# Optimization experiments

Hardware: AMD Instinct MI355X
Metric: run time of the kernel (lower is better)

## Reference

```python
import jax, jax.numpy as jnp
import numpy as np

HEAD_SIZE = 64
N_EMBED = 768
B, T = 16, 2048


def setup_inputs() -> dict:
    key = jax.random.key(0)
    ks = jax.random.split(key, 7)
    return {
        "x": jax.random.normal(ks[0], (B, T, N_EMBED), dtype=jnp.float32),
        "v1": jax.random.normal(ks[1], (B, T, HEAD_SIZE), dtype=jnp.float32),
        "Wk": jax.random.normal(ks[2], (N_EMBED, HEAD_SIZE), dtype=jnp.float32) * 0.02,
        "Wq": jax.random.normal(ks[3], (N_EMBED, HEAD_SIZE), dtype=jnp.float32) * 0.02,
        "Wv": jax.random.normal(ks[4], (N_EMBED, HEAD_SIZE), dtype=jnp.float32) * 0.02,
        "Wproj": jax.random.normal(ks[5], (HEAD_SIZE, HEAD_SIZE), dtype=jnp.float32) * 0.02,
        "bproj": jnp.zeros((HEAD_SIZE,), dtype=jnp.float32),
        "lamb": jnp.float32(0.5),
    }


def reference(x, v1, Wk, Wq, Wv, Wproj, bproj, lamb):
    # x: [B, T, C]; single-head causal attention with value-residual mixing.
    k = x @ Wk  # [B, T, H]
    q = x @ Wq
    v = x @ Wv
    v = (1.0 - lamb) * v + lamb * v1  # value-residual mix
    scale = jnp.float32(1.0 / np.sqrt(HEAD_SIZE))
    w = jnp.einsum("bth,bsh->bts", q, k) * scale  # [B, T, T]
    t = x.shape[1]
    causal = jnp.tril(jnp.ones((t, t), dtype=bool))  # [T, T]
    w = jnp.where(causal, w, jnp.float32(-jnp.inf))
    w = jax.nn.softmax(w, axis=-1)
    # dropout is identity in eval mode
    out = jnp.einsum("bts,bsh->bth", w, v)  # [B, T, H]
    return out @ Wproj + bproj, v1
```

## Files before the change

kernel.cpp:

```cpp
#include <hip/hip_runtime.h>
#include <hip/hip_bf16.h>


constexpr int BATCH = 16;
constexpr int TSEQ  = 2048;
constexpr int CEMB  = 768;
constexpr int HS    = 64;
constexpr size_t NTOK    = (size_t)BATCH * TSEQ;
constexpr size_t OUTHALF = NTOK * HS;

typedef __bf16 bf16x4 __attribute__((ext_vector_type(4)));
typedef __bf16 bf16x8 __attribute__((ext_vector_type(8)));
typedef float  f32x4  __attribute__((ext_vector_type(4)));
typedef float  f32x16 __attribute__((ext_vector_type(16)));
typedef int    i32x4  __attribute__((ext_vector_type(4)));

__global__ __launch_bounds__(256) void prep_kernel(
    const float* __restrict__ wk, const float* __restrict__ wq,
    const float* __restrict__ wv, const float* __restrict__ wproj,
    __bf16* __restrict__ wt, __bf16* __restrict__ wpt)
{
    __shared__ __bf16 t[64][66];
    const int bid = blockIdx.x;
    if (bid < 36) {
        const int m = bid / 12, c0 = (bid % 12) * 64;
        const float* src = (m == 0) ? wk : (m == 1) ? wq : wv;
        for (int i = threadIdx.x; i < 4096; i += 256) {
            const int c = i >> 6, h = i & 63;
            t[c][h] = (__bf16)src[(size_t)(c0 + c) * HS + h];
        }
        __syncthreads();
        for (int i = threadIdx.x; i < 4096; i += 256) {
            const int h = i >> 6, c = i & 63;
            wt[(size_t)m * HS * CEMB + (size_t)h * CEMB + c0 + c] = t[c][h];
        }
    } else {
        for (int i = threadIdx.x; i < 4096; i += 256) {
            const int h = i >> 6, hp = i & 63;
            t[h][hp] = (__bf16)wproj[i];
        }
        __syncthreads();
        for (int i = threadIdx.x; i < 4096; i += 256) {
            const int hp = i >> 6, h = i & 63;
            wpt[i] = t[h][hp];
        }
    }
}

__global__ __launch_bounds__(256, 2) void qkv_kernel(
    const float* __restrict__ x,
    const float* __restrict__ v1,
    const __bf16* __restrict__ wt,
    const float* __restrict__ lamb_p,
    __bf16* __restrict__ kk,
    __bf16* __restrict__ qq,
    __bf16* __restrict__ vt,
    float* __restrict__ v1out)
{
    __shared__ __bf16 xl[2][64][88];

    const int wave = threadIdx.x >> 6;
    const int lane = threadIdx.x & 63;
    const int l16  = lane & 15;
    const int quad = lane >> 4;
    const size_t row0 = (size_t)blockIdx.x * 64;

    const int tok_s = threadIdx.x >> 2;
    const int cq    = threadIdx.x & 3;
    const float* xsrc = x + (row0 + tok_s) * CEMB + cq * 16;

    const __bf16* wbase[3];
    #pragma unroll
    for (int m = 0; m < 3; ++m)
        wbase[m] = wt + ((size_t)m * HS + wave * 16 + l16) * CEMB + quad * 8;

    f32x4 acc[3][4];
    #pragma unroll
    for (int m = 0; m < 3; ++m)
        #pragma unroll
        for (int rt = 0; rt < 4; ++rt)
            acc[m][rt] = (f32x4){0.f, 0.f, 0.f, 0.f};

    auto issueX = [&](int chunk, f32x4& a0, f32x4& a1, f32x4& a2, f32x4& a3) {
        const float* xs = xsrc + chunk * 64;
        a0 = *(const f32x4*)(xs);
        a1 = *(const f32x4*)(xs + 4);
        a2 = *(const f32x4*)(xs + 8);
        a3 = *(const f32x4*)(xs + 12);
    };
    auto writeX = [&](int buf, const f32x4& a0, const f32x4& a1,
                      const f32x4& a2, const f32x4& a3) {
        bf16x8 lo, hi;
        #pragma unroll
        for (int i = 0; i < 4; ++i) {
            lo[i] = (__bf16)a0[i]; lo[i + 4] = (__bf16)a1[i];
            hi[i] = (__bf16)a2[i]; hi[i + 4] = (__bf16)a3[i];
        }
        *(bf16x8*)&xl[buf][tok_s][cq * 16]     = lo;
        *(bf16x8*)&xl[buf][tok_s][cq * 16 + 8] = hi;
    };
    auto loadW = [&](int chunk, bf16x8 (&w)[3][2]) {
        #pragma unroll
        for (int m = 0; m < 3; ++m)
            #pragma unroll
            for (int ks = 0; ks < 2; ++ks)
                w[m][ks] = *(const bf16x8*)(wbase[m] + chunk * 64 + ks * 32);
    };
    auto compute = [&](int buf, const bf16x8 (&w)[3][2]) {
        #pragma unroll
        for (int ks = 0; ks < 2; ++ks) {
            bf16x8 a[4];
            #pragma unroll
            for (int rt = 0; rt < 4; ++rt)
                a[rt] = *(const bf16x8*)&xl[buf][rt * 16 + l16][ks * 32 + quad * 8];
            #pragma unroll
            for (int m = 0; m < 3; ++m)
                #pragma unroll
                for (int rt = 0; rt < 4; ++rt)
                    acc[m][rt] = __builtin_amdgcn_mfma_f32_16x16x32_bf16(
                        a[rt], w[m][ks], acc[m][rt], 0, 0, 0);
        }
    };

    f32x4 xa0, xa1, xa2, xa3, xb0, xb1, xb2, xb3;
    {
        f32x4 t0, t1, t2, t3;
        issueX(0, t0, t1, t2, t3);
        writeX(0, t0, t1, t2, t3);
    }
    issueX(1, xa0, xa1, xa2, xa3);
    issueX(2, xb0, xb1, xb2, xb3);
    bf16x8 wcur[3][2], wnxt[3][2];
    loadW(0, wcur);
    __syncthreads();

    constexpr int NCH = CEMB / 64;
    #pragma unroll
    for (int ci = 0; ci < NCH; ci += 2) {
        loadW(ci + 1, wnxt);
        compute(0, wcur);
        writeX(1, xa0, xa1, xa2, xa3);
        if (ci + 3 < NCH) issueX(ci + 3, xa0, xa1, xa2, xa3);
        __syncthreads();

        if (ci + 2 < NCH) loadW(ci + 2, wcur);
        compute(1, wnxt);
        if (ci + 2 < NCH) {
            writeX(0, xb0, xb1, xb2, xb3);
            if (ci + 4 < NCH) issueX(ci + 4, xb0, xb1, xb2, xb3);
            __syncthreads();
        }
    }

    const float lam = lamb_p[0];
    const int col = wave * 16 + l16;
    const int b  = (int)(row0 >> 11);
    __bf16* vtb = vt + (size_t)b * HS * TSEQ + (size_t)col * TSEQ;
    #pragma unroll
    for (int rt = 0; rt < 4; ++rt) {
        const size_t tok0 = row0 + rt * 16 + quad * 4;
        bf16x4 pk;
        #pragma unroll
        for (int r = 0; r < 4; ++r) {
            const size_t idx = (tok0 + r) * HS + col;
            const float v1v = v1[idx];
            kk[idx] = (__bf16)acc[0][rt][r];
            qq[idx] = (__bf16)acc[1][rt][r];
            pk[r] = (__bf16)((1.0f - lam) * acc[2][rt][r] + lam * v1v);
            if (v1out) v1out[idx] = v1v;
        }
        *(bf16x4*)(vtb + (tok0 & 2047)) = pk;
    }
}

__device__ __forceinline__ int pk2(float lo, float hi) {
    unsigned short a = __builtin_bit_cast(unsigned short, (__bf16)lo);
    unsigned short b = __builtin_bit_cast(unsigned short, (__bf16)hi);
    return (int)((((unsigned)b) << 16) | (unsigned)a);
}
__device__ __forceinline__ bf16x8 make_bfrag(const float* p, int hi) {
    const int a0 = pk2(p[0], p[1]), a1 = pk2(p[2], p[3]);
    const int b0 = pk2(p[4], p[5]), b1 = pk2(p[6], p[7]);
    const int pa0 = __shfl_xor(a0, 32), pa1 = __shfl_xor(a1, 32);
    const int pb0 = __shfl_xor(b0, 32), pb1 = __shfl_xor(b1, 32);
    i32x4 w;
    w[0] = hi ? pb0 : a0;
    w[1] = hi ? pb1 : a1;
    w[2] = hi ? b0  : pa0;
    w[3] = hi ? b1  : pa1;
    return __builtin_bit_cast(bf16x8, w);
}

__global__ __launch_bounds__(256, 2) void attn_kernel(
    const __bf16* __restrict__ q,
    const __bf16* __restrict__ k,
    const __bf16* __restrict__ vt,
    const __bf16* __restrict__ wpt,
    const float* __restrict__ bproj,
    float* __restrict__ y)
{
    __shared__ float olds[4][64][32];
    __shared__ float mred[4][32];
    __shared__ float lred[4][32];

    const int b    = blockIdx.x >> 5;
    const int jp   = blockIdx.x & 31;
    const int wave = threadIdx.x >> 6;
    const int lane = threadIdx.x & 63;
    const int l31  = lane & 31;
    const int hi   = lane >> 5;
    const int hi8  = hi * 8;

    const __bf16* kb = k  + (size_t)b * TSEQ * HS;
    const __bf16* vb = vt + (size_t)b * HS * TSEQ;
    const float sc2 = 0.125f * 1.44269504f;

    bf16x8 wf[4];
    if (wave < 2) {
        const __bf16* wp = wpt + (size_t)(wave * 32 + l31) * HS + hi8;
        #pragma unroll
        for (int c = 0; c < 4; ++c) wf[c] = *(const bf16x8*)(wp + c * 16);
    }

    for (int pass = 0; pass < 2; ++pass) {
        const int j = pass ? (63 - jp) : jp;
        const size_t tok0 = (size_t)b * TSEQ + (size_t)j * 32;

        const __bf16* qp = q + (tok0 + l31) * HS + hi8;
        bf16x8 qf[4];
        #pragma unroll
        for (int c = 0; c < 4; ++c) qf[c] = *(const bf16x8*)(qp + c * 16);

        f32x16 o0, o1;
        #pragma unroll
        for (int r = 0; r < 16; ++r) { o0[r] = 0.f; o1[r] = 0.f; }
        float m_i = -1e30f, l_i = 0.f;

        bf16x8 kf[4], kn[4];
        if (wave <= j) {
            const __bf16* kp = kb + (size_t)(wave * 32 + l31) * HS + hi8;
            #pragma unroll
            for (int c = 0; c < 4; ++c) kf[c] = *(const bf16x8*)(kp + c * 16);
        }

        for (int t = wave; t <= j; t += 4) {
            const int s0 = t * 32;
            bf16x8 vf[4];
            #pragma unroll
            for (int ht = 0; ht < 2; ++ht)
                #pragma unroll
                for (int c2 = 0; c2 < 2; ++c2)
                    vf[ht * 2 + c2] = *(const bf16x8*)(vb
                        + (size_t)(ht * 32 + l31) * TSEQ + s0 + c2 * 16 + hi8);
            if (t + 4 <= j) {
                const __bf16* kp = kb + (size_t)((t + 4) * 32 + l31) * HS + hi8;
                #pragma unroll
                for (int c = 0; c < 4; ++c) kn[c] = *(const bf16x8*)(kp + c * 16);
            }

            f32x16 s;
            #pragma unroll
            for (int r = 0; r < 16; ++r) s[r] = 0.f;
            #pragma unroll
            for (int c = 0; c < 4; ++c)
                s = __builtin_amdgcn_mfma_f32_32x32x16_bf16(kf[c], qf[c], s, 0, 0, 0);

            float p[16];
            if (t == j) {
                #pragma unroll
                for (int r = 0; r < 16; ++r) {
                    const int krow = (r & 3) + 8 * (r >> 2) + 4 * hi;
                    p[r] = (krow <= l31) ? s[r] * sc2 : -1e30f;
                }
            } else {
                #pragma unroll
                for (int r = 0; r < 16; ++r) p[r] = s[r] * sc2;
            }

            float x0 = fmaxf(p[0], p[1]),   x1 = fmaxf(p[2], p[3]);
            float x2 = fmaxf(p[4], p[5]),   x3 = fmaxf(p[6], p[7]);
            float x4 = fmaxf(p[8], p[9]),   x5 = fmaxf(p[10], p[11]);
            float x6 = fmaxf(p[12], p[13]), x7 = fmaxf(p[14], p[15]);
            float mx = fmaxf(fmaxf(fmaxf(x0, x1), fmaxf(x2, x3)),
                             fmaxf(fmaxf(x4, x5), fmaxf(x6, x7)));
            mx = fmaxf(mx, __shfl_xor(mx, 32));

            if (!__all(mx <= m_i + 8.f)) {
                const float mn = fmaxf(m_i, mx);
                const float alpha = exp2f(m_i - mn);
                m_i = mn;
                l_i *= alpha;
                #pragma unroll
                for (int r = 0; r < 16; ++r) { o0[r] *= alpha; o1[r] *= alpha; }
            }

            #pragma unroll
            for (int r = 0; r < 16; ++r) p[r] = exp2f(p[r] - m_i);

            float r0 = (p[0] + p[1]) + (p[2] + p[3]);
            float r1 = (p[4] + p[5]) + (p[6] + p[7]);
            float r2 = (p[8] + p[9]) + (p[10] + p[11]);
            float r3 = (p[12] + p[13]) + (p[14] + p[15]);
            float rs = (r0 + r1) + (r2 + r3);
            rs += __shfl_xor(rs, 32);
            l_i += rs;

            const bf16x8 fb0 = make_bfrag(&p[0], hi);
            const bf16x8 fb1 = make_bfrag(&p[8], hi);

            o0 = __builtin_amdgcn_mfma_f32_32x32x16_bf16(vf[0], fb0, o0, 0, 0, 0);
            o0 = __builtin_amdgcn_mfma_f32_32x32x16_bf16(vf[1], fb1, o0, 0, 0, 0);
            o1 = __builtin_amdgcn_mfma_f32_32x32x16_bf16(vf[2], fb0, o1, 0, 0, 0);
            o1 = __builtin_amdgcn_mfma_f32_32x32x16_bf16(vf[3], fb1, o1, 0, 0, 0);

            if (t + 4 <= j) {
                #pragma unroll
                for (int c = 0; c < 4; ++c) kf[c] = kn[c];
            }
        }

        #pragma unroll
        for (int r = 0; r < 16; ++r) {
            const int row = (r & 3) + 8 * (r >> 2) + 4 * hi;
            olds[wave][row][l31]      = o0[r];
            olds[wave][row + 32][l31] = o1[r];
        }
        if (lane < 32) { mred[wave][lane] = m_i; lred[wave][lane] = l_i; }
        __syncthreads();

        if (wave < 2) {
            float mw[4], lw[4];
            #pragma unroll
            for (int w = 0; w < 4; ++w) { mw[w] = mred[w][l31]; lw[w] = lred[w][l31]; }
            const float mg = fmaxf(fmaxf(mw[0], mw[1]), fmaxf(mw[2], mw[3]));
            float g[4], lg = 0.f;
            #pragma unroll
            for (int w = 0; w < 4; ++w) { g[w] = exp2f(mw[w] - mg); lg += g[w] * lw[w]; }
            const float inv = 1.0f / lg;

            float on[32];
            #pragma unroll
            for (int r = 0; r < 16; ++r) {
                const int row = (r & 3) + 8 * (r >> 2) + 4 * hi;
                float a0 = 0.f, a1 = 0.f;
                #pragma unroll
                for (int w = 0; w < 4; ++w) {
                    a0 += g[w] * olds[w][row][l31];
                    a1 += g[w] * olds[w][row + 32][l31];
                }
                on[r]      = a0 * inv;
                on[r + 16] = a1 * inv;
            }

            f32x16 res;
            #pragma unroll
            for (int r = 0; r < 16; ++r) res[r] = 0.f;
            #pragma unroll
            for (int c = 0; c < 4; ++c) {
                const bf16x8 ob = make_bfrag(&on[c * 8], hi);
                res = __builtin_amdgcn_mfma_f32_32x32x16_bf16(wf[c], ob, res, 0, 0, 0);
            }

            float* yp = y + (tok0 + l31) * HS + wave * 32;
            #pragma unroll
            for (int grp = 0; grp < 4; ++grp) {
                const f32x4 bb = *(const f32x4*)(bproj + wave * 32 + grp * 8 + 4 * hi);
                f32x4 o4;
                #pragma unroll
                for (int rr = 0; rr < 4; ++rr) o4[rr] = res[grp * 4 + rr] + bb[rr];
                *(f32x4*)(yp + grp * 8 + 4 * hi) = o4;
            }
        }
        __syncthreads();
    }
}

__global__ __launch_bounds__(256) void copy_kernel(
    const float* __restrict__ src, float* __restrict__ dst)
{
    const size_t i = ((size_t)blockIdx.x * 256 + threadIdx.x) * 4;
    *(f32x4*)(dst + i) = *(const f32x4*)(src + i);
}

extern "C" void kernel_launch(void* const* d_in, const int* in_sizes, int n_in,
                              void* d_out, int out_size, void* d_ws, size_t ws_size,
                              hipStream_t stream) {
    const float* x     = (const float*)d_in[0];
    const float* v1    = (const float*)d_in[1];
    const float* wk    = (const float*)d_in[2];
    const float* wq    = (const float*)d_in[3];
    const float* wv    = (const float*)d_in[4];
    const float* wproj = (const float*)d_in[5];
    const float* bproj = (const float*)d_in[6];
    const float* lamb  = (const float*)d_in[7];

    float* out = (float*)d_out;

    __bf16* qp  = (__bf16*)d_ws;
    __bf16* wt  = qp + OUTHALF;
    __bf16* wpt = wt + (size_t)3 * HS * CEMB;
    const size_t base_elems = OUTHALF + (size_t)3 * HS * CEMB + (size_t)HS * HS;
    const size_t need_bytes = (base_elems + 2 * OUTHALF) * sizeof(__bf16);

    __bf16* kp;
    __bf16* vtp;
    float*  v1out;
    const bool fused_v1 = (ws_size >= need_bytes);
    if (fused_v1) {
        kp    = wpt + (size_t)HS * HS;
        vtp   = kp + OUTHALF;
        v1out = out + OUTHALF;
    } else {
        kp    = (__bf16*)(out + OUTHALF);
        vtp   = kp + OUTHALF;
        v1out = nullptr;
    }

    prep_kernel<<<dim3(37), dim3(256), 0, stream>>>(wk, wq, wv, wproj, wt, wpt);

    qkv_kernel<<<dim3((int)(NTOK / 64)), dim3(256), 0, stream>>>(
        x, v1, wt, lamb, kp, qp, vtp, v1out);

    attn_kernel<<<dim3(BATCH * 32), dim3(256), 0, stream>>>(
        qp, kp, vtp, wpt, bproj, out);

    if (!fused_v1) {
        copy_kernel<<<dim3((int)(OUTHALF / (256 * 4))), dim3(256), 0, stream>>>(
            v1, out + OUTHALF);
    }
}
```

Before: 229.4 us.

## Split QKV projection across grid.y so each block computes one matrix

The QKV projection kernel launches three blocks per 64-token tile, one each for K, Q and V, instead of one block computing all three. This cuts accumulator and weight registers so the launch bound can allow four blocks per CU, and the x pipeline becomes a simpler single-stage double buffer. In exchange, the fp32 x activations are read and converted three times instead of once, which raises global memory traffic unless the cache absorbs the repeats.

Result: slower. 250.0 us (+9.0%).

```diff
diff --git a/kernel.cpp b/kernel.cpp
--- a/kernel.cpp
+++ b/kernel.cpp
@@ -47,7 +47,7 @@
     }
 }
 
-__global__ __launch_bounds__(256, 2) void qkv_kernel(
+__global__ __launch_bounds__(256, 4) void qkv_kernel(
     const float* __restrict__ x,
     const float* __restrict__ v1,
     const __bf16* __restrict__ wt,
@@ -59,6 +59,7 @@
 {
     __shared__ __bf16 xl[2][64][88];
 
+    const int mm   = blockIdx.y;
     const int wave = threadIdx.x >> 6;
     const int lane = threadIdx.x & 63;
     const int l16  = lane & 15;
@@ -69,17 +70,11 @@
     const int cq    = threadIdx.x & 3;
     const float* xsrc = x + (row0 + tok_s) * CEMB + cq * 16;
 
-    const __bf16* wbase[3];
+    const __bf16* wb = wt + ((size_t)mm * HS + wave * 16 + l16) * CEMB + quad * 8;
+
+    f32x4 acc[4];
     #pragma unroll
-    for (int m = 0; m < 3; ++m)
-        wbase[m] = wt + ((size_t)m * HS + wave * 16 + l16) * CEMB + quad * 8;
-
-    f32x4 acc[3][4];
-    #pragma unroll
-    for (int m = 0; m < 3; ++m)
-        #pragma unroll
-        for (int rt = 0; rt < 4; ++rt)
-            acc[m][rt] = (f32x4){0.f, 0.f, 0.f, 0.f};
+    for (int rt = 0; rt < 4; ++rt) acc[rt] = (f32x4){0.f, 0.f, 0.f, 0.f};
 
     auto issueX = [&](int chunk, f32x4& a0, f32x4& a1, f32x4& a2, f32x4& a3) {
         const float* xs = xsrc + chunk * 64;
@@ -99,77 +94,84 @@
         *(bf16x8*)&xl[buf][tok_s][cq * 16]     = lo;
         *(bf16x8*)&xl[buf][tok_s][cq * 16 + 8] = hi;
     };
-    auto loadW = [&](int chunk, bf16x8 (&w)[3][2]) {
-        #pragma unroll
-        for (int m = 0; m < 3; ++m)
-            #pragma unroll
-            for (int ks = 0; ks < 2; ++ks)
-                w[m][ks] = *(const bf16x8*)(wbase[m] + chunk * 64 + ks * 32);
-    };
-    auto compute = [&](int buf, const bf16x8 (&w)[3][2]) {
-        #pragma unroll
-        for (int ks = 0; ks < 2; ++ks) {
-            bf16x8 a[4];
-            #pragma unroll
-            for (int rt = 0; rt < 4; ++rt)
-                a[rt] = *(const bf16x8*)&xl[buf][rt * 16 + l16][ks * 32 + quad * 8];
-            #pragma unroll
-            for (int m = 0; m < 3; ++m)
-                #pragma unroll
-                for (int rt = 0; rt < 4; ++rt)
-                    acc[m][rt] = __builtin_amdgcn_mfma_f32_16x16x32_bf16(
-                        a[rt], w[m][ks], acc[m][rt], 0, 0, 0);
-        }
-    };
-
-    f32x4 xa0, xa1, xa2, xa3, xb0, xb1, xb2, xb3;
+
     {
         f32x4 t0, t1, t2, t3;
         issueX(0, t0, t1, t2, t3);
         writeX(0, t0, t1, t2, t3);
     }
+    f32x4 xa0, xa1, xa2, xa3;
     issueX(1, xa0, xa1, xa2, xa3);
-    issueX(2, xb0, xb1, xb2, xb3);
-    bf16x8 wcur[3][2], wnxt[3][2];
-    loadW(0, wcur);
+    bf16x8 wc0 = *(const bf16x8*)(wb);
+    bf16x8 wc1 = *(const bf16x8*)(wb + 32);
     __syncthreads();
 
     constexpr int NCH = CEMB / 64;
     #pragma unroll
-    for (int ci = 0; ci < NCH; ci += 2) {
-        loadW(ci + 1, wnxt);
-        compute(0, wcur);
-        writeX(1, xa0, xa1, xa2, xa3);
-        if (ci + 3 < NCH) issueX(ci + 3, xa0, xa1, xa2, xa3);
-        __syncthreads();
-
-        if (ci + 2 < NCH) loadW(ci + 2, wcur);
-        compute(1, wnxt);
-        if (ci + 2 < NCH) {
-            writeX(0, xb0, xb1, xb2, xb3);
-            if (ci + 4 < NCH) issueX(ci + 4, xb0, xb1, xb2, xb3);
+    for (int ci = 0; ci < NCH; ++ci) {
+        const int buf = ci & 1;
+        const bool notlast = (ci + 1 < NCH);
+
+        bf16x8 wn0, wn1;
+        if (notlast) {
+            wn0 = *(const bf16x8*)(wb + (ci + 1) * 64);
+            wn1 = *(const bf16x8*)(wb + (ci + 1) * 64 + 32);
+        }
+
+        #pragma unroll
+        for (int ks = 0; ks < 2; ++ks) {
+            const bf16x8 w = ks ? wc1 : wc0;
+            #pragma unroll
+            for (int rt = 0; rt < 4; ++rt) {
+                const bf16x8 a = *(const bf16x8*)
+                    &xl[buf][rt * 16 + l16][ks * 32 + quad * 8];
+                acc[rt] = __builtin_amdgcn_mfma_f32_16x16x32_bf16(
+                    a, w, acc[rt], 0, 0, 0);
+            }
+        }
+
+        if (notlast) {
+            writeX(buf ^ 1, xa0, xa1, xa2, xa3);
+            if (ci + 2 < NCH) issueX(ci + 2, xa0, xa1, xa2, xa3);
+            wc0 = wn0; wc1 = wn1;
             __syncthreads();
         }
     }
 
-    const float lam = lamb_p[0];
     const int col = wave * 16 + l16;
-    const int b  = (int)(row0 >> 11);
-    __bf16* vtb = vt + (size_t)b * HS * TSEQ + (size_t)col * TSEQ;
-    #pragma unroll
-    for (int rt = 0; rt < 4; ++rt) {
-        const size_t tok0 = row0 + rt * 16 + quad * 4;
-        bf16x4 pk;
-        #pragma unroll
-        for (int r = 0; r < 4; ++r) {
-            const size_t idx = (tok0 + r) * HS + col;
-            const float v1v = v1[idx];
-            kk[idx] = (__bf16)acc[0][rt][r];
-            qq[idx] = (__bf16)acc[1][rt][r];
-            pk[r] = (__bf16)((1.0f - lam) * acc[2][rt][r] + lam * v1v);
-            if (v1out) v1out[idx] = v1v;
-        }
-        *(bf16x4*)(vtb + (tok0 & 2047)) = pk;
+    if (mm == 0) {
+        #pragma unroll
+        for (int rt = 0; rt < 4; ++rt) {
+            const size_t tok0 = row0 + rt * 16 + quad * 4;
+            #pragma unroll
+            for (int r = 0; r < 4; ++r)
+                kk[(tok0 + r) * HS + col] = (__bf16)acc[rt][r];
+        }
+    } else if (mm == 1) {
+        #pragma unroll
+        for (int rt = 0; rt < 4; ++rt) {
+            const size_t tok0 = row0 + rt * 16 + quad * 4;
+            #pragma unroll
+            for (int r = 0; r < 4; ++r)
+                qq[(tok0 + r) * HS + col] = (__bf16)acc[rt][r];
+        }
+    } else {
+        const float lam = lamb_p[0];
+        const int b = (int)(row0 >> 11);
+        __bf16* vtb = vt + (size_t)b * HS * TSEQ + (size_t)col * TSEQ;
+        #pragma unroll
+        for (int rt = 0; rt < 4; ++rt) {
+            const size_t tok0 = row0 + rt * 16 + quad * 4;
+            bf16x4 pk;
+            #pragma unroll
+            for (int r = 0; r < 4; ++r) {
+                const size_t idx = (tok0 + r) * HS + col;
+                const float v1v = v1[idx];
+                pk[r] = (__bf16)((1.0f - lam) * acc[rt][r] + lam * v1v);
+                if (v1out) v1out[idx] = v1v;
+            }
+            *(bf16x4*)(vtb + (tok0 & 2047)) = pk;
+        }
     }
 }
 
@@ -418,7 +420,7 @@
 
     prep_kernel<<<dim3(37), dim3(256), 0, stream>>>(wk, wq, wv, wproj, wt, wpt);
 
-    qkv_kernel<<<dim3((int)(NTOK / 64)), dim3(256), 0, stream>>>(
+    qkv_kernel<<<dim3((int)(NTOK / 64), 3), dim3(256), 0, stream>>>(
         x, v1, wt, lamb, kp, qp, vtp, v1out);
 
     attn_kernel<<<dim3(BATCH * 32), dim3(256), 0, stream>>>(
```

## Stage x tiles into LDS with direct global_load_lds in the QKV projection

Applied to the files above, without the earlier changes.

The QKV projection kernel now copies fp32 x chunks straight from global memory into shared memory using global_load_lds, rather than loading into registers, converting to bf16 and storing to LDS. The bf16 conversion moves to the point where MFMA operands are read from LDS. The pipeline becomes a double buffer with one chunk per iteration and a single sync, which frees registers and removes the register round trip. In exchange the LDS footprint doubles because fp32 is stored, LDS read traffic doubles, and conversion work is repeated on every operand read.

Result: no change. 228.0 us (-0.6%).

```diff
diff --git a/kernel.cpp b/kernel.cpp
--- a/kernel.cpp
+++ b/kernel.cpp
@@ -57,7 +57,7 @@
     __bf16* __restrict__ vt,
     float* __restrict__ v1out)
 {
-    __shared__ __bf16 xl[2][64][88];
+    __shared__ float xf[2][64][68];
 
     const int wave = threadIdx.x >> 6;
     const int lane = threadIdx.x & 63;
@@ -65,10 +65,6 @@
     const int quad = lane >> 4;
     const size_t row0 = (size_t)blockIdx.x * 64;
 
-    const int tok_s = threadIdx.x >> 2;
-    const int cq    = threadIdx.x & 3;
-    const float* xsrc = x + (row0 + tok_s) * CEMB + cq * 16;
-
     const __bf16* wbase[3];
     #pragma unroll
     for (int m = 0; m < 3; ++m)
@@ -81,23 +77,16 @@
         for (int rt = 0; rt < 4; ++rt)
             acc[m][rt] = (f32x4){0.f, 0.f, 0.f, 0.f};
 
-    auto issueX = [&](int chunk, f32x4& a0, f32x4& a1, f32x4& a2, f32x4& a3) {
-        const float* xs = xsrc + chunk * 64;
-        a0 = *(const f32x4*)(xs);
-        a1 = *(const f32x4*)(xs + 4);
-        a2 = *(const f32x4*)(xs + 8);
-        a3 = *(const f32x4*)(xs + 12);
-    };
-    auto writeX = [&](int buf, const f32x4& a0, const f32x4& a1,
-                      const f32x4& a2, const f32x4& a3) {
-        bf16x8 lo, hi;
-        #pragma unroll
-        for (int i = 0; i < 4; ++i) {
-            lo[i] = (__bf16)a0[i]; lo[i + 4] = (__bf16)a1[i];
-            hi[i] = (__bf16)a2[i]; hi[i + 4] = (__bf16)a3[i];
-        }
-        *(bf16x8*)&xl[buf][tok_s][cq * 16]     = lo;
-        *(bf16x8*)&xl[buf][tok_s][cq * 16 + 8] = hi;
+    auto stage = [&](int buf, int chunk) {
+        #pragma unroll
+        for (int i = 0; i < 16; ++i) {
+            const int tok = i * 4 + wave;
+            const float* g = x + (row0 + tok) * CEMB + chunk * 64 + lane;
+            __builtin_amdgcn_global_load_lds(
+                (const __attribute__((address_space(1))) unsigned*)g,
+                (__attribute__((address_space(3))) unsigned*)&xf[buf][tok][0],
+                4, 0, 0);
+        }
     };
     auto loadW = [&](int chunk, bf16x8 (&w)[3][2]) {
         #pragma unroll
@@ -111,8 +100,17 @@
         for (int ks = 0; ks < 2; ++ks) {
             bf16x8 a[4];
             #pragma unroll
-            for (int rt = 0; rt < 4; ++rt)
-                a[rt] = *(const bf16x8*)&xl[buf][rt * 16 + l16][ks * 32 + quad * 8];
+            for (int rt = 0; rt < 4; ++rt) {
+                const float* p = &xf[buf][rt * 16 + l16][ks * 32 + quad * 8];
+                const f32x4 u0 = *(const f32x4*)p;
+                const f32x4 u1 = *(const f32x4*)(p + 4);
+                bf16x8 r;
+                #pragma unroll
+                for (int j = 0; j < 4; ++j) {
+                    r[j] = (__bf16)u0[j]; r[j + 4] = (__bf16)u1[j];
+                }
+                a[rt] = r;
+            }
             #pragma unroll
             for (int m = 0; m < 3; ++m)
                 #pragma unroll
@@ -122,33 +120,26 @@
         }
     };
 
-    f32x4 xa0, xa1, xa2, xa3, xb0, xb1, xb2, xb3;
-    {
-        f32x4 t0, t1, t2, t3;
-        issueX(0, t0, t1, t2, t3);
-        writeX(0, t0, t1, t2, t3);
-    }
-    issueX(1, xa0, xa1, xa2, xa3);
-    issueX(2, xb0, xb1, xb2, xb3);
-    bf16x8 wcur[3][2], wnxt[3][2];
-    loadW(0, wcur);
+    stage(0, 0);
+    stage(1, 1);
+    bf16x8 wc[3][2], wn[3][2];
+    loadW(0, wc);
     __syncthreads();
 
     constexpr int NCH = CEMB / 64;
     #pragma unroll
-    for (int ci = 0; ci < NCH; ci += 2) {
-        loadW(ci + 1, wnxt);
-        compute(0, wcur);
-        writeX(1, xa0, xa1, xa2, xa3);
-        if (ci + 3 < NCH) issueX(ci + 3, xa0, xa1, xa2, xa3);
-        __syncthreads();
-
-        if (ci + 2 < NCH) loadW(ci + 2, wcur);
-        compute(1, wnxt);
-        if (ci + 2 < NCH) {
-            writeX(0, xb0, xb1, xb2, xb3);
-            if (ci + 4 < NCH) issueX(ci + 4, xb0, xb1, xb2, xb3);
+    for (int ci = 0; ci < NCH; ++ci) {
+        const int buf = ci & 1;
+        const bool notlast = (ci + 1 < NCH);
+        if (notlast) loadW(ci + 1, wn);
+        compute(buf, wc);
+        if (notlast) {
+            #pragma unroll
+            for (int m = 0; m < 3; ++m)
+                #pragma unroll
+                for (int ks = 0; ks < 2; ++ks) wc[m][ks] = wn[m][ks];
             __syncthreads();
+            if (ci + 2 < NCH) stage(buf, ci + 2);
         }
     }
 
```
